# Optimization experiments

Hardware: AMD Instinct MI355X
Metric: run time of the kernel (lower is better)

## Reference

```python
import jax, jax.numpy as jnp
import numpy as np

SEQ_LEN = 128
INPUT_SIZE = 512
HIDDEN_SIZE = 1024
MEAN_DIM = 3
COV_DIM = 6
HEAD_DIM = 128


def setup_inputs() -> dict:
    key = jax.random.key(0)
    ks = jax.random.split(key, 16)
    B, I, H = 256, INPUT_SIZE, HIDDEN_SIZE
    s_i = 1.0 / np.sqrt(H)
    inp = {
        "encoder_outputs": jax.random.normal(ks[0], (B, 64, H), jnp.float32),
        "encoder_hidden": jax.random.normal(ks[1], (1, B, H), jnp.float32),
        # GRU weights (PyTorch layout: gates ordered r,z,n along dim 0)
        "W_ih": jax.random.uniform(ks[2], (3 * H, I), jnp.float32, -s_i, s_i),
        "W_hh": jax.random.uniform(ks[3], (3 * H, H), jnp.float32, -s_i, s_i),
        "b_ih": jax.random.uniform(ks[4], (3 * H,), jnp.float32, -s_i, s_i),
        "b_hh": jax.random.uniform(ks[5], (3 * H,), jnp.float32, -s_i, s_i),
        # out: Linear(H -> I)
        "W_out": jax.random.uniform(ks[6], (I, H), jnp.float32, -s_i, s_i),
        "b_out": jax.random.uniform(ks[7], (I,), jnp.float32, -s_i, s_i),
        # mean head: I -> 128 -> meanDim
        "Wm1": jax.random.uniform(ks[8], (HEAD_DIM, I), jnp.float32, -1/np.sqrt(I), 1/np.sqrt(I)),
        "bm1": jax.random.uniform(ks[9], (HEAD_DIM,), jnp.float32, -1/np.sqrt(I), 1/np.sqrt(I)),
        "Wm2": jax.random.uniform(ks[10], (MEAN_DIM, HEAD_DIM), jnp.float32, -1/np.sqrt(HEAD_DIM), 1/np.sqrt(HEAD_DIM)),
        "bm2": jax.random.uniform(ks[11], (MEAN_DIM,), jnp.float32, -1/np.sqrt(HEAD_DIM), 1/np.sqrt(HEAD_DIM)),
        # cov head: I -> 128 -> covDim
        "Wc1": jax.random.uniform(ks[12], (HEAD_DIM, I), jnp.float32, -1/np.sqrt(I), 1/np.sqrt(I)),
        "bc1": jax.random.uniform(ks[13], (HEAD_DIM,), jnp.float32, -1/np.sqrt(I), 1/np.sqrt(I)),
        "Wc2": jax.random.uniform(ks[14], (COV_DIM, HEAD_DIM), jnp.float32, -1/np.sqrt(HEAD_DIM), 1/np.sqrt(HEAD_DIM)),
        "bc2": jax.random.uniform(ks[15], (COV_DIM,), jnp.float32, -1/np.sqrt(HEAD_DIM), 1/np.sqrt(HEAD_DIM)),
    }
    return inp


def _gru_decode(x0, h0, W_ih, W_hh, b_ih, b_hh, W_out, b_out):
    def step(carry, _):
        x, h = carry
        xr = jax.nn.relu(x)                          # relu(input.float())
        gi = xr @ W_ih.T + b_ih                      # [B, 3H]
        gh = h @ W_hh.T + b_hh                       # [B, 3H]
        ir, iz, inn = jnp.split(gi, 3, axis=-1)
        hr, hz, hn = jnp.split(gh, 3, axis=-1)
        r = jax.nn.sigmoid(ir + hr)
        z = jax.nn.sigmoid(iz + hz)
        n = jnp.tanh(inn + r * hn)
        h_new = (1.0 - z) * n + z * h
        out = h_new @ W_out.T + b_out                # [B, I]
        return (jax.lax.stop_gradient(out), h_new), out

    (_, _), outs = jax.lax.scan(step, (x0, h0), None, length=SEQ_LEN)
    return jnp.transpose(outs, (1, 0, 2))            # [B, S, I]


def reference(encoder_outputs, encoder_hidden, W_ih, W_hh, b_ih, b_hh,
              W_out, b_out, Wm1, bm1, Wm2, bm2, Wc1, bc1, Wc2, bc2):
    B = encoder_outputs.shape[0]
    h0 = encoder_hidden[0]                           # [B, H]
    x0 = jnp.zeros((B, INPUT_SIZE), jnp.float32)     # deterministic init (torch.empty in orig)
    outs = _gru_decode(x0, h0, W_ih, W_hh, b_ih, b_hh, W_out, b_out)
    means = jax.nn.relu(outs @ Wm1.T + bm1) @ Wm2.T + bm2
    covs = jax.nn.relu(outs @ Wc1.T + bc1) @ Wc2.T + bc2
    return means, covs
```

## Files before the change

kernel.cpp:

```cpp
#include <hip/hip_runtime.h>


#define HID 1024
#define INP 512
#define BATCH 256
#define SEQ 128
#define NWG 256
#define NTHR 256
#define WIH_LD 520
#define WHH_LD 1032

typedef _Float16 f16x8 __attribute__((ext_vector_type(8)));
typedef float f32x4 __attribute__((ext_vector_type(4)));

__device__ __forceinline__ float fast_sigmoid(float x) {
    return 1.0f / (1.0f + __expf(-x));
}
__device__ __forceinline__ float fast_tanh(float x) {
    return 1.0f - 2.0f / (__expf(2.0f * x) + 1.0f);
}

struct Params {
    const float *ehid, *Wih, *Whh, *bih, *bhh, *Wout, *bout;
    const float *Wm1, *bm1, *Wm2, *bm2, *Wc1, *bc1, *Wc2, *bc2;
    _Float16 *WoutH, *Wm1H, *Wc1H;
    float *h32; _Float16 *h16; _Float16 *outs;
    int *bar; float *dout;
};

__device__ __forceinline__ void gbar(int* bar) {
    __syncthreads();
    if (threadIdx.x == 0) {
        int g = __hip_atomic_load(bar + 32, __ATOMIC_RELAXED, __HIP_MEMORY_SCOPE_AGENT);
        int a = __hip_atomic_fetch_add(bar, 1, __ATOMIC_RELEASE, __HIP_MEMORY_SCOPE_AGENT);
        if (a == NWG - 1) {
            __hip_atomic_store(bar, 0, __ATOMIC_RELAXED, __HIP_MEMORY_SCOPE_AGENT);
            __hip_atomic_fetch_add(bar + 32, 1, __ATOMIC_RELEASE, __HIP_MEMORY_SCOPE_AGENT);
        } else {
            while (__hip_atomic_load(bar + 32, __ATOMIC_RELAXED, __HIP_MEMORY_SCOPE_AGENT) == g) {
                __builtin_amdgcn_s_sleep(2);
            }
        }
        __builtin_amdgcn_fence(__ATOMIC_ACQUIRE, "agent");
    }
    __syncthreads();
}

__global__ __launch_bounds__(NTHR, 1) void gru_persistent(Params p) {
    __shared__ __align__(16) char smraw[3 * 16 * WIH_LD * 2 + 3 * 16 * WHH_LD * 2];
    __shared__ float red[2 * 16 * 16];
    _Float16* wih_s = (_Float16*)smraw;
    _Float16* whh_s = (_Float16*)(smraw + 3 * 16 * WIH_LD * 2);
    _Float16* hid_s = (_Float16*)smraw;

    const int w = blockIdx.x;
    const int wave = threadIdx.x >> 6;
    const int lane = threadIdx.x & 63;
    const int l15 = lane & 15;
    const int kq = lane >> 4;

    {
        const int tid = w * NTHR + threadIdx.x;
        const int nth = NWG * NTHR;
        for (int i = tid; i < INP * HID / 4; i += nth) {
            float4 v = ((const float4*)p.Wout)[i];
            _Float16* d = p.WoutH + i * 4;
            d[0] = (_Float16)v.x; d[1] = (_Float16)v.y; d[2] = (_Float16)v.z; d[3] = (_Float16)v.w;
        }
        for (int i = tid; i < 128 * INP / 4; i += nth) {
            float4 v = ((const float4*)p.Wm1)[i];
            _Float16* d = p.Wm1H + i * 4;
            d[0] = (_Float16)v.x; d[1] = (_Float16)v.y; d[2] = (_Float16)v.z; d[3] = (_Float16)v.w;
            float4 u = ((const float4*)p.Wc1)[i];
            _Float16* e = p.Wc1H + i * 4;
            e[0] = (_Float16)u.x; e[1] = (_Float16)u.y; e[2] = (_Float16)u.z; e[3] = (_Float16)u.w;
        }
        for (int i = tid; i < BATCH * HID / 4; i += nth) {
            float4 v = ((const float4*)p.ehid)[i];
            ((float4*)p.h32)[i] = v;
            _Float16* d = p.h16 + i * 4;
            d[0] = (_Float16)v.x; d[1] = (_Float16)v.y; d[2] = (_Float16)v.z; d[3] = (_Float16)v.w;
        }
    }

    const int jj = w >> 2;
    const int b4 = w & 3;
    for (int i = threadIdx.x; i < 3 * 16 * (INP / 4); i += NTHR) {
        int gi = i / (16 * (INP / 4));
        int rr = (i / (INP / 4)) % 16;
        int kk = (i % (INP / 4)) * 4;
        float4 v = *(const float4*)(p.Wih + ((size_t)(gi * HID + jj * 16 + rr)) * INP + kk);
        _Float16* d = &wih_s[(gi * 16 + rr) * WIH_LD + kk];
        d[0] = (_Float16)v.x; d[1] = (_Float16)v.y; d[2] = (_Float16)v.z; d[3] = (_Float16)v.w;
    }
    for (int i = threadIdx.x; i < 3 * 16 * (HID / 4); i += NTHR) {
        int gi = i / (16 * (HID / 4));
        int rr = (i / (HID / 4)) % 16;
        int kk = (i % (HID / 4)) * 4;
        float4 v = *(const float4*)(p.Whh + ((size_t)(gi * HID + jj * 16 + rr)) * HID + kk);
        _Float16* d = &whh_s[(gi * 16 + rr) * WHH_LD + kk];
        d[0] = (_Float16)v.x; d[1] = (_Float16)v.y; d[2] = (_Float16)v.z; d[3] = (_Float16)v.w;
    }

    gbar(p.bar);

    const int jc = jj * 16 + l15;
    const float brr = p.bih[jc] + p.bhh[jc];
    const float bzz = p.bih[HID + jc] + p.bhh[HID + jc];
    const float bin = p.bih[2 * HID + jc];
    const float bhn = p.bhh[2 * HID + jc];
    const int grow  = b4 * 64 + wave * 16 + l15;
    const int gcrow = b4 * 64 + wave * 16 + kq * 4;

    const int ort = w >> 4;
    const int oct = w & 15;
    const int csub = wave & 1;
    const int khalf = wave >> 1;
    const int orow = ort * 16 + l15;
    const int ocol = oct * 32 + csub * 16 + l15;
    const float obout = p.bout[ocol];

    for (int t = 0; t < SEQ; ++t) {
        const int cur = t & 1, nxt = 1 - cur;
        const float*    h32p = p.h32 + (size_t)cur * BATCH * HID;
        float*          h32n = p.h32 + (size_t)nxt * BATCH * HID;
        const _Float16* h16p = p.h16 + (size_t)cur * BATCH * HID;
        _Float16*       h16n = p.h16 + (size_t)nxt * BATCH * HID;

        f32x4 ar = {0.f,0.f,0.f,0.f}, az = {0.f,0.f,0.f,0.f};
        f32x4 ai = {0.f,0.f,0.f,0.f}, ah = {0.f,0.f,0.f,0.f};
        if (t > 0) {
            const _Float16* xp = p.outs + ((size_t)grow * SEQ + (t - 1)) * INP + kq * 8;
            #pragma unroll 4
            for (int kk = 0; kk < INP; kk += 32) {
                f16x8 a = *(const f16x8*)(xp + kk);
                #pragma unroll
                for (int q = 0; q < 8; ++q) a[q] = a[q] > (_Float16)0.f ? a[q] : (_Float16)0.f;
                f16x8 br = *(const f16x8*)&wih_s[(0 * 16 + l15) * WIH_LD + kk + kq * 8];
                f16x8 bz = *(const f16x8*)&wih_s[(1 * 16 + l15) * WIH_LD + kk + kq * 8];
                f16x8 bn = *(const f16x8*)&wih_s[(2 * 16 + l15) * WIH_LD + kk + kq * 8];
                ar = __builtin_amdgcn_mfma_f32_16x16x32_f16(a, br, ar, 0, 0, 0);
                az = __builtin_amdgcn_mfma_f32_16x16x32_f16(a, bz, az, 0, 0, 0);
                ai = __builtin_amdgcn_mfma_f32_16x16x32_f16(a, bn, ai, 0, 0, 0);
            }
        }
        {
            const _Float16* hp = h16p + (size_t)grow * HID + kq * 8;
            #pragma unroll 4
            for (int kk = 0; kk < HID; kk += 32) {
                f16x8 a = *(const f16x8*)(hp + kk);
                f16x8 br = *(const f16x8*)&whh_s[(0 * 16 + l15) * WHH_LD + kk + kq * 8];
                f16x8 bz = *(const f16x8*)&whh_s[(1 * 16 + l15) * WHH_LD + kk + kq * 8];
                f16x8 bn = *(const f16x8*)&whh_s[(2 * 16 + l15) * WHH_LD + kk + kq * 8];
                ar = __builtin_amdgcn_mfma_f32_16x16x32_f16(a, br, ar, 0, 0, 0);
                az = __builtin_amdgcn_mfma_f32_16x16x32_f16(a, bz, az, 0, 0, 0);
                ah = __builtin_amdgcn_mfma_f32_16x16x32_f16(a, bn, ah, 0, 0, 0);
            }
        }
        #pragma unroll
        for (int i = 0; i < 4; ++i) {
            int r = gcrow + i;
            float rr = fast_sigmoid(ar[i] + brr);
            float zz = fast_sigmoid(az[i] + bzz);
            float nn = fast_tanh(ai[i] + bin + rr * (ah[i] + bhn));
            float hold = h32p[(size_t)r * HID + jc];
            float hv = (1.0f - zz) * nn + zz * hold;
            h32n[(size_t)r * HID + jc] = hv;
            h16n[(size_t)r * HID + jc] = (_Float16)hv;
        }

        gbar(p.bar);

        {
            f32x4 acc = {0.f,0.f,0.f,0.f};
            const _Float16* ap = h16n + (size_t)orow * HID + khalf * 512 + kq * 8;
            const _Float16* bp = p.WoutH + (size_t)ocol * HID + khalf * 512 + kq * 8;
            #pragma unroll 4
            for (int kk = 0; kk < 512; kk += 32) {
                f16x8 a = *(const f16x8*)(ap + kk);
                f16x8 b = *(const f16x8*)(bp + kk);
                acc = __builtin_amdgcn_mfma_f32_16x16x32_f16(a, b, acc, 0, 0, 0);
            }
            if (khalf == 1) {
                #pragma unroll
                for (int i = 0; i < 4; ++i)
                    red[(csub * 16 + kq * 4 + i) * 16 + l15] = acc[i];
            }
            __syncthreads();
            if (khalf == 0) {
                #pragma unroll
                for (int i = 0; i < 4; ++i) {
                    float v = acc[i] + red[(csub * 16 + kq * 4 + i) * 16 + l15];
                    p.outs[((size_t)(ort * 16 + kq * 4 + i) * SEQ + t) * INP + ocol] =
                        (_Float16)(v + obout);
                }
            }
        }

        gbar(p.bar);
    }

    {
        const int b = w;
        const size_t rowbase = (size_t)b * SEQ;
        for (int head = 0; head < 2; ++head) {
            const _Float16* W1 = head ? p.Wc1H : p.Wm1H;
            const float* b1 = head ? p.bc1 : p.bm1;
            f32x4 acc[2][8];
            #pragma unroll
            for (int rf = 0; rf < 2; ++rf)
                #pragma unroll
                for (int ct = 0; ct < 8; ++ct) acc[rf][ct] = (f32x4){0.f,0.f,0.f,0.f};
            for (int kk = 0; kk < INP; kk += 32) {
                f16x8 a0 = *(const f16x8*)(p.outs + (rowbase + wave * 32 + l15) * INP + kk + kq * 8);
                f16x8 a1 = *(const f16x8*)(p.outs + (rowbase + wave * 32 + 16 + l15) * INP + kk + kq * 8);
                #pragma unroll
                for (int ct = 0; ct < 8; ++ct) {
                    f16x8 bb = *(const f16x8*)(W1 + (size_t)(ct * 16 + l15) * INP + kk + kq * 8);
                    acc[0][ct] = __builtin_amdgcn_mfma_f32_16x16x32_f16(a0, bb, acc[0][ct], 0, 0, 0);
                    acc[1][ct] = __builtin_amdgcn_mfma_f32_16x16x32_f16(a1, bb, acc[1][ct], 0, 0, 0);
                }
            }
            __syncthreads();
            #pragma unroll
            for (int rf = 0; rf < 2; ++rf) {
                int rl = wave * 32 + rf * 16 + kq * 4;
                #pragma unroll
                for (int ct = 0; ct < 8; ++ct) {
                    int col = ct * 16 + l15;
                    float bb1 = b1[col];
                    #pragma unroll
                    for (int i = 0; i < 4; ++i) {
                        float v = acc[rf][ct][i] + bb1;
                        hid_s[(rl + i) * 136 + col] = (_Float16)(v > 0.f ? v : 0.f);
                    }
                }
            }
            __syncthreads();
            if (threadIdx.x < 128) {
                int srow = threadIdx.x;
                if (head == 0) {
                    float a0 = p.bm2[0], a1 = p.bm2[1], a2 = p.bm2[2];
                    for (int k = 0; k < 128; ++k) {
                        float hv = (float)hid_s[srow * 136 + k];
                        a0 += hv * p.Wm2[k];
                        a1 += hv * p.Wm2[128 + k];
                        a2 += hv * p.Wm2[256 + k];
                    }
                    size_t o = ((size_t)b * 128 + srow) * 3;
                    p.dout[o] = a0; p.dout[o + 1] = a1; p.dout[o + 2] = a2;
                } else {
                    float a[6];
                    #pragma unroll
                    for (int m = 0; m < 6; ++m) a[m] = p.bc2[m];
                    for (int k = 0; k < 128; ++k) {
                        float hv = (float)hid_s[srow * 136 + k];
                        #pragma unroll
                        for (int m = 0; m < 6; ++m) a[m] += hv * p.Wc2[m * 128 + k];
                    }
                    size_t o = (size_t)BATCH * SEQ * 3 + ((size_t)b * 128 + srow) * 6;
                    #pragma unroll
                    for (int m = 0; m < 6; ++m) p.dout[o + m] = a[m];
                }
            }
            __syncthreads();
        }
    }
}

extern "C" void kernel_launch(void* const* d_in, const int* in_sizes, int n_in,
                              void* d_out, int out_size, void* d_ws, size_t ws_size,
                              hipStream_t stream) {
    (void)in_sizes; (void)n_in; (void)out_size; (void)ws_size;
    Params prm;
    prm.ehid = (const float*)d_in[1];
    prm.Wih  = (const float*)d_in[2];
    prm.Whh  = (const float*)d_in[3];
    prm.bih  = (const float*)d_in[4];
    prm.bhh  = (const float*)d_in[5];
    prm.Wout = (const float*)d_in[6];
    prm.bout = (const float*)d_in[7];
    prm.Wm1  = (const float*)d_in[8];
    prm.bm1  = (const float*)d_in[9];
    prm.Wm2  = (const float*)d_in[10];
    prm.bm2  = (const float*)d_in[11];
    prm.Wc1  = (const float*)d_in[12];
    prm.bc1  = (const float*)d_in[13];
    prm.Wc2  = (const float*)d_in[14];
    prm.bc2  = (const float*)d_in[15];
    prm.dout = (float*)d_out;

    char* ws = (char*)d_ws;
    prm.bar   = (int*)ws;
    prm.WoutH = (_Float16*)(ws + 256);
    prm.Wm1H  = (_Float16*)(ws + 256 + 1048576);
    prm.Wc1H  = (_Float16*)(ws + 256 + 1179648);
    prm.h32   = (float*)   (ws + 256 + 1310720);
    prm.h16   = (_Float16*)(ws + 256 + 3407872);
    prm.outs  = (_Float16*)(ws + 256 + 4456448);

    hipMemsetAsync(ws, 0, 256, stream);
    void* args[] = { &prm };
    hipLaunchCooperativeKernel((void*)gru_persistent, dim3(NWG), dim3(NTHR),
                               args, 0, stream);
}
```

Baseline: 4.078 ms.

## Replace grid-wide barriers with per-batch-group flag synchronization in GRU loop

Swaps the two global atomic barriers per timestep for per-workgroup progress flags. Each workgroup waits only on the 64 producers in its batch group: the hidden-state producers before the output projection, and the output producers before the next gate step. This removes all-to-all barrier serialization and lets batch groups advance independently, at the cost of 64-lane polling of flag arrays and more complex memory ordering.

```diff
diff --git a/kernel.cpp b/kernel.cpp
--- a/kernel.cpp
+++ b/kernel.cpp
@@ -25,7 +25,7 @@
     const float *Wm1, *bm1, *Wm2, *bm2, *Wc1, *bc1, *Wc2, *bc2;
     _Float16 *WoutH, *Wm1H, *Wc1H;
     float *h32; _Float16 *h16; _Float16 *outs;
-    int *bar; float *dout;
+    int *bar; int *flagA; int *flagB; float *dout;
 };
 
 __device__ __forceinline__ void gbar(int* bar) {
@@ -46,6 +46,22 @@
     __syncthreads();
 }
 
+__device__ __forceinline__ void wait_flags64(const int* flags, int target) {
+    const int lane = threadIdx.x & 63;
+    while (true) {
+        int v = __hip_atomic_load(flags + lane, __ATOMIC_RELAXED, __HIP_MEMORY_SCOPE_AGENT);
+        if (!__any(v < target)) break;
+        __builtin_amdgcn_s_sleep(1);
+    }
+    __builtin_amdgcn_fence(__ATOMIC_ACQUIRE, "agent");
+}
+
+__device__ __forceinline__ void set_flag(int* flag, int val) {
+    __syncthreads();
+    if (threadIdx.x == 0)
+        __hip_atomic_store(flag, val, __ATOMIC_RELEASE, __HIP_MEMORY_SCOPE_AGENT);
+}
+
 __global__ __launch_bounds__(NTHR, 1) void gru_persistent(Params p) {
     __shared__ __align__(16) char smraw[3 * 16 * WIH_LD * 2 + 3 * 16 * WHH_LD * 2];
     __shared__ float red[2 * 16 * 16];
@@ -114,11 +130,17 @@
 
     const int ort = w >> 4;
     const int oct = w & 15;
+    const int og  = w >> 6;
     const int csub = wave & 1;
     const int khalf = wave >> 1;
     const int orow = ort * 16 + l15;
     const int ocol = oct * 32 + csub * 16 + l15;
     const float obout = p.bout[ocol];
+
+    int* myFlagA = p.flagA + b4 * 64 + jj;
+    int* myFlagB = p.flagB + og * 64 + (ort & 3) * 16 + oct;
+    const int* grpFlagB = p.flagB + b4 * 64;
+    const int* grpFlagA = p.flagA + og * 64;
 
     for (int t = 0; t < SEQ; ++t) {
         const int cur = t & 1, nxt = 1 - cur;
@@ -126,6 +148,8 @@
         float*          h32n = p.h32 + (size_t)nxt * BATCH * HID;
         const _Float16* h16p = p.h16 + (size_t)cur * BATCH * HID;
         _Float16*       h16n = p.h16 + (size_t)nxt * BATCH * HID;
+
+        if (t > 0) wait_flags64(grpFlagB, t);
 
         f32x4 ar = {0.f,0.f,0.f,0.f}, az = {0.f,0.f,0.f,0.f};
         f32x4 ai = {0.f,0.f,0.f,0.f}, ah = {0.f,0.f,0.f,0.f};
@@ -169,8 +193,9 @@
             h16n[(size_t)r * HID + jc] = (_Float16)hv;
         }
 
-        gbar(p.bar);
-
+        set_flag(myFlagA, t + 1);
+
+        wait_flags64(grpFlagA, t + 1);
         {
             f32x4 acc = {0.f,0.f,0.f,0.f};
             const _Float16* ap = h16n + (size_t)orow * HID + khalf * 512 + kq * 8;
@@ -197,11 +222,12 @@
             }
         }
 
-        gbar(p.bar);
+        set_flag(myFlagB, t + 1);
     }
 
     {
         const int b = w;
+        wait_flags64(p.flagB + (b >> 6) * 64, SEQ);
         const size_t rowbase = (size_t)b * SEQ;
         for (int head = 0; head < 2; ++head) {
             const _Float16* W1 = head ? p.Wc1H : p.Wm1H;
@@ -292,14 +318,16 @@
 
     char* ws = (char*)d_ws;
     prm.bar   = (int*)ws;
-    prm.WoutH = (_Float16*)(ws + 256);
-    prm.Wm1H  = (_Float16*)(ws + 256 + 1048576);
-    prm.Wc1H  = (_Float16*)(ws + 256 + 1179648);
-    prm.h32   = (float*)   (ws + 256 + 1310720);
-    prm.h16   = (_Float16*)(ws + 256 + 3407872);
-    prm.outs  = (_Float16*)(ws + 256 + 4456448);
-
-    hipMemsetAsync(ws, 0, 256, stream);
+    prm.flagA = (int*)(ws + 256);
+    prm.flagB = (int*)(ws + 1280);
+    prm.WoutH = (_Float16*)(ws + 4096);
+    prm.Wm1H  = (_Float16*)(ws + 4096 + 1048576);
+    prm.Wc1H  = (_Float16*)(ws + 4096 + 1179648);
+    prm.h32   = (float*)   (ws + 4096 + 1310720);
+    prm.h16   = (_Float16*)(ws + 4096 + 3407872);
+    prm.outs  = (_Float16*)(ws + 4096 + 4456448);
+
+    hipMemsetAsync(ws, 0, 2304, stream);
     void* args[] = { &prm };
     hipLaunchCooperativeKernel((void*)gru_persistent, dim3(NWG), dim3(NTHR),
                                args, 0, stream);
```

After: 5.707 ms. +39.9%, slower.
